# Kernel optimization log

Measured on AMD Instinct MI355X. Metric: run time of the kernel, lower is better.

Reference implementation:

```python
import jax, jax.numpy as jnp
import numpy as np


def _grid_sample_bilinear(img, grid):
    # img: [B,C,H,W]; grid: [B,Hg,Wg,2] normalized to [-1,1] (x,y), align_corners=False,
    # zero padding (torch F.grid_sample defaults).
    B, C, H, W = img.shape
    Hg, Wg = grid.shape[1], grid.shape[2]
    gx, gy = grid[..., 0], grid[..., 1]
    ix = (gx + 1.0) * (W * 0.5) - 0.5
    iy = (gy + 1.0) * (H * 0.5) - 0.5
    ix0 = jnp.floor(ix)
    iy0 = jnp.floor(iy)
    tx = (ix - ix0).reshape(B, 1, -1)
    ty = (iy - iy0).reshape(B, 1, -1)
    img_flat = img.reshape(B, C, H * W)

    def corner(xi, yi):
        valid = ((xi >= 0) & (xi < W) & (yi >= 0) & (yi < H)).reshape(B, 1, -1)
        xc = jnp.clip(xi, 0, W - 1).astype(jnp.int32)
        yc = jnp.clip(yi, 0, H - 1).astype(jnp.int32)
        idx = (yc * W + xc).reshape(B, -1)                      # [B, Hg*Wg]
        vals = jax.vmap(lambda f, i: f[:, i])(img_flat, idx)    # [B, C, Hg*Wg]
        return vals * valid

    v00 = corner(ix0, iy0)
    v01 = corner(ix0 + 1, iy0)
    v10 = corner(ix0, iy0 + 1)
    v11 = corner(ix0 + 1, iy0 + 1)
    out = (v00 * (1 - tx) * (1 - ty) + v01 * tx * (1 - ty)
           + v10 * (1 - tx) * ty + v11 * tx * ty)
    return out.reshape(B, C, Hg, Wg)


def setup_inputs() -> dict:
    key = jax.random.key(0)
    ks = jax.random.split(key, 8)
    B, C, RHO, WP = 32, 384, 25, 256
    HC, WC = 64, 64
    D = 2 * C  # 768, channels after polar/cart concat
    std = 0.02
    return {
        "polar_feat": jax.random.normal(ks[0], (B, C, RHO, WP), jnp.float32),
        "cart_feat": jax.random.normal(ks[1], (B, C, HC, WC), jnp.float32),
        "grid": jax.random.uniform(ks[2], (B, RHO, WP, 2), jnp.float32, -1.0, 1.0),
        "W1_0": jax.random.normal(ks[3], (D, 40), jnp.float32) * std,
        "b1_0": jnp.zeros((40,), jnp.float32),
        "W2_0": jax.random.normal(ks[4], (40, 1), jnp.float32) * std,
        "b2_0": jnp.zeros((1,), jnp.float32),
        "W1s": jax.random.normal(ks[5], (24, D + 1, 40), jnp.float32) * std,
        "b1s": jnp.zeros((24, 40), jnp.float32),
        "W2s": jax.random.normal(ks[6], (24, 40, 1), jnp.float32) * std,
        "b2s": jnp.zeros((24, 1), jnp.float32),
    }


def reference(polar_feat, cart_feat, grid, W1_0, b1_0, W2_0, b2_0, W1s, b1s, W2s, b2s):
    # Polar grid-sample fusion of cartesian features onto the polar grid.
    fe_cart_p = _grid_sample_bilinear(cart_feat, grid)              # [B,C,25,Wp]
    fe_cat_p = jnp.concatenate([polar_feat, fe_cart_p], axis=1)     # [B,768,25,Wp]
    # AdaptiveAvgPool2d((None,1)): mean over width.
    fe = jnp.mean(fe_cat_p, axis=3)                                 # [B,768,25]

    feats = jnp.transpose(fe, (2, 0, 1))                            # [25,B,768]
    gelu = lambda x: jax.nn.gelu(x, approximate=False)

    # Head 0: no recurrent input.
    h0 = gelu(feats[0] @ W1_0 + b1_0)
    out0 = h0 @ W2_0 + b2_0                                         # [B,1]

    # Heads 1..24: concat previous scalar output before first linear (fully_local=False).
    def step(out_prev, xs):
        feat, W1, b1, W2, b2 = xs
        x = jnp.concatenate([feat, out_prev], axis=-1)              # [B,769]
        h = gelu(x @ W1 + b1)
        o = h @ W2 + b2                                             # [B,1]
        return o, o

    _, outs = jax.lax.scan(step, out0, (feats[1:], W1s, b1s, W2s, b2s))
    out = jnp.concatenate([out0[None], outs], axis=0)               # [25,B,1]
    out = jnp.transpose(out[:, :, 0], (1, 0))                       # [B,25]
    return jnp.clip(out, 0.0, jnp.pi)
```

## Files before the change

### kernel.cpp

```cpp
#include <hip/hip_runtime.h>
#include <math.h>

#define B_    32
#define C_    384
#define RHO_  25
#define WP_   256
#define PIX_  4096
#define D_    768
#define HID_  40
#define NROWS (B_*C_*RHO_)
#define FE_N (RHO_*B_*D_)
#define POLARBLK 2048
#define PCH 8
#define WFRAG_B 262144

typedef _Float16 half_t;
typedef __attribute__((ext_vector_type(8))) _Float16 half8;
typedef __attribute__((ext_vector_type(4))) float f32x4;

__device__ __forceinline__ float gelu_exact(float x) {
    return 0.5f * x * (1.f + erff(x * 0.70710678118654752f));
}

__global__ __launch_bounds__(256) void front_kernel(const float* __restrict__ polar,
        const float* __restrict__ grid,
        const float* __restrict__ W1_0, const float* __restrict__ W1s,
        half_t* __restrict__ Wfrag, float* __restrict__ W1T, float* __restrict__ fe) {
    __shared__ float lb[PIX_];
    int tid = threadIdx.x;
    int bid = blockIdx.x;
    if (bid < POLARBLK) {
        int wid = bid * 4 + (tid >> 6);
        int lane = tid & 63;
        const int NW = POLARBLK * 4;
        for (int r0 = wid; r0 < NROWS; r0 += 4 * NW) {
            float s[4];
            #pragma unroll
            for (int k = 0; k < 4; ++k) {
                int r = r0 + k * NW;
                float4 v = (r < NROWS) ? ((const float4*)(polar + (size_t)r * WP_))[lane]
                                       : make_float4(0.f, 0.f, 0.f, 0.f);
                s[k] = v.x + v.y + v.z + v.w;
            }
            #pragma unroll
            for (int m = 32; m >= 1; m >>= 1) {
                #pragma unroll
                for (int k = 0; k < 4; ++k) s[k] += __shfl_xor(s[k], m, 64);
            }
            if (lane == 0) {
                #pragma unroll
                for (int k = 0; k < 4; ++k) {
                    int r = r0 + k * NW;
                    if (r < NROWS) {
                        int rho = r % RHO_, cch = (r / RHO_) % C_, bb = r / (RHO_ * C_);
                        fe[((size_t)(rho * B_ + bb)) * D_ + cch] = s[k] * (1.f / 256.f);
                    }
                }
            }
        }
    } else if (bid < POLARBLK + B_ * RHO_) {
        int bb = bid - POLARBLK;
        for (int i = tid; i < PIX_ / 4; i += 256) ((float4*)lb)[i] = make_float4(0.f, 0.f, 0.f, 0.f);
        __syncthreads();
        int pt = bb * WP_ + tid;
        float2 g = ((const float2*)grid)[pt];
        float ix = (g.x + 1.f) * 32.f - 0.5f;
        float iy = (g.y + 1.f) * 32.f - 0.5f;
        float x0f = floorf(ix), y0f = floorf(iy);
        float fx = ix - x0f, fy = iy - y0f;
        int x0 = (int)x0f, y0 = (int)y0f;
        const float s = 1.f / 256.f;
        if ((unsigned)x0 < 64u) {
            if ((unsigned)y0 < 64u)       atomicAdd(&lb[y0 * 64 + x0],       (1.f - fx) * (1.f - fy) * s);
            if ((unsigned)(y0 + 1) < 64u) atomicAdd(&lb[(y0 + 1) * 64 + x0], (1.f - fx) * fy * s);
        }
        if ((unsigned)(x0 + 1) < 64u) {
            if ((unsigned)y0 < 64u)       atomicAdd(&lb[y0 * 64 + x0 + 1],       fx * (1.f - fy) * s);
            if ((unsigned)(y0 + 1) < 64u) atomicAdd(&lb[(y0 + 1) * 64 + x0 + 1], fx * fy * s);
        }
        __syncthreads();
        int b = bb / RHO_, rho = bb % RHO_;
        int slot_h = (rho < 16) ? 0 : 1;
        int r16 = rho & 15;
        half_t* base = Wfrag + (size_t)b * WFRAG_B;
        for (int i = tid; i < PIX_; i += 256) {
            int t = i >> 5, k = i & 31;
            int kg = k >> 3, ii = k & 7;
            float wv = lb[i];
            half_t h = (half_t)wv;
            size_t idx = ((size_t)(t * 4 + slot_h) * 64 + kg * 16 + r16) * 8 + ii;
            base[idx] = h;
            base[idx + 1024] = (half_t)(wv - (float)h);
        }
    } else if (bid < POLARBLK + B_ * RHO_ + 25) {
        int i = bid - (POLARBLK + B_ * RHO_);
        const float* src = (i == 0) ? W1_0 : (W1s + (size_t)(i - 1) * 769 * HID_);
        float* dst = W1T + (size_t)i * HID_ * D_;
        for (int idx = tid; idx < HID_ * D_; idx += 256) {
            int j = idx / D_, c = idx % D_;
            dst[idx] = src[c * HID_ + j];
        }
    } else {
        int z = bid - (POLARBLK + B_ * RHO_ + 25);
        for (int i = tid; i < 16 * 96; i += 256) {
            int row = z * 16 + (i / 96), e = i % 96;
            ((float4*)fe)[(size_t)row * 192 + 96 + e] = make_float4(0.f, 0.f, 0.f, 0.f);
        }
    }
}

__global__ __launch_bounds__(256) void cart_mfma_kernel(const float* __restrict__ cart,
        const half_t* __restrict__ Wfrag, float* __restrict__ fe) {
    __shared__ float smem[8704];
    int tid = threadIdx.x;
    int bid = blockIdx.x;
    int b  = bid / (6 * PCH);
    int ct = (bid / PCH) % 6;
    int pc = bid % PCH;
    int w = tid >> 6, lane = tid & 63;
    int row16 = lane & 15, kg = lane >> 4;

    const float* xgbase = cart + ((size_t)b * C_ + ct * 64 + w * 16) * PIX_ + pc * 512;
    const half_t* wbase = Wfrag + (size_t)b * WFRAG_B + (size_t)(pc * 16) * 2048 + lane * 8;

    float* xl = smem + w * 2176;
    int srow = lane >> 4;
    int scol = (lane & 15) * 4;

    f32x4 acc0 = {0.f, 0.f, 0.f, 0.f};
    f32x4 acc1 = {0.f, 0.f, 0.f, 0.f};
    float4 sreg[4];
    half8 wf[2][8];

    #pragma unroll
    for (int i = 0; i < 4; ++i)
        sreg[i] = *(const float4*)(xgbase + (size_t)(srow + 4 * i) * PIX_ + scol);
    #pragma unroll
    for (int ks = 0; ks < 2; ++ks)
        #pragma unroll
        for (int s = 0; s < 4; ++s)
            wf[0][ks * 4 + s] = *(const half8*)(wbase + (size_t)(ks * 4 + s) * 512);
    #pragma unroll
    for (int i = 0; i < 4; ++i)
        *(float4*)(&xl[(srow + 4 * i) * 68 + scol]) = sreg[i];
    #pragma unroll
    for (int i = 0; i < 4; ++i)
        sreg[i] = *(const float4*)(xgbase + (size_t)(srow + 4 * i) * PIX_ + 64 + scol);
    #pragma unroll
    for (int ks = 0; ks < 2; ++ks)
        #pragma unroll
        for (int s = 0; s < 4; ++s)
            wf[1][ks * 4 + s] = *(const half8*)(wbase + (size_t)((2 + ks) * 4 + s) * 512);

    #pragma unroll
    for (int t = 0; t < 8; ++t) {
        const int cb = t & 1;
        const float* xb = xl + cb * 1088;
        #pragma unroll
        for (int ks = 0; ks < 2; ++ks) {
            float4 xa = *(const float4*)(xb + row16 * 68 + ks * 32 + kg * 8);
            float4 xc = *(const float4*)(xb + row16 * 68 + ks * 32 + kg * 8 + 4);
            float xs[8] = {xa.x, xa.y, xa.z, xa.w, xc.x, xc.y, xc.z, xc.w};
            half8 ah, al;
            #pragma unroll
            for (int i = 0; i < 8; ++i) {
                half_t h = (half_t)xs[i];
                ah[i] = h;
                al[i] = (half_t)(xs[i] - (float)h);
            }
            acc0 = __builtin_amdgcn_mfma_f32_16x16x32_f16(ah, wf[cb][ks * 4 + 0], acc0, 0, 0, 0);
            acc0 = __builtin_amdgcn_mfma_f32_16x16x32_f16(ah, wf[cb][ks * 4 + 2], acc0, 0, 0, 0);
            acc0 = __builtin_amdgcn_mfma_f32_16x16x32_f16(al, wf[cb][ks * 4 + 0], acc0, 0, 0, 0);
            acc1 = __builtin_amdgcn_mfma_f32_16x16x32_f16(ah, wf[cb][ks * 4 + 1], acc1, 0, 0, 0);
            acc1 = __builtin_amdgcn_mfma_f32_16x16x32_f16(ah, wf[cb][ks * 4 + 3], acc1, 0, 0, 0);
            acc1 = __builtin_amdgcn_mfma_f32_16x16x32_f16(al, wf[cb][ks * 4 + 1], acc1, 0, 0, 0);
        }
        if (t < 7) {
            #pragma unroll
            for (int i = 0; i < 4; ++i)
                *(float4*)(&xl[(cb ^ 1) * 1088 + (srow + 4 * i) * 68 + scol]) = sreg[i];
            if (t < 6) {
                int off = (t + 2) * 64;
                #pragma unroll
                for (int i = 0; i < 4; ++i)
                    sreg[i] = *(const float4*)(xgbase + (size_t)(srow + 4 * i) * PIX_ + off + scol);
                #pragma unroll
                for (int ks = 0; ks < 2; ++ks)
                    #pragma unroll
                    for (int s = 0; s < 4; ++s)
                        wf[cb][ks * 4 + s] = *(const half8*)(wbase + (size_t)(((t + 2) * 2 + ks) * 4 + s) * 512);
            }
        }
    }

    __syncthreads();
    #pragma unroll
    for (int r = 0; r < 4; ++r)
        smem[row16 * 64 + w * 16 + kg * 4 + r] = acc0[r];
    int rho1 = 16 + row16;
    if (rho1 < RHO_) {
        #pragma unroll
        for (int r = 0; r < 4; ++r)
            smem[rho1 * 64 + w * 16 + kg * 4 + r] = acc1[r];
    }
    __syncthreads();
    for (int oi = tid; oi < 1600; oi += 256) {
        int r = oi >> 6, cc = oi & 63;
        atomicAdd(&fe[((size_t)(r * B_ + b)) * D_ + 384 + ct * 64 + cc], smem[oi]);
    }
}

__global__ __launch_bounds__(256) void mlp_pre_kernel(const float* __restrict__ fe,
        const float* __restrict__ W1T, const float* __restrict__ b1_0,
        const float* __restrict__ b1s, float* __restrict__ G) {
    int lane = threadIdx.x & 63;
    int trip = blockIdx.x * 4 + (threadIdx.x >> 6);
    int jh = trip & 1;
    int pair = trip >> 1;
    int i = pair >> 5, b = pair & 31;
    const float4* f4p = (const float4*)(fe + (size_t)(i * B_ + b) * D_);
    float4 f0 = f4p[lane], f1 = f4p[lane + 64], f2 = f4p[lane + 128];
    int j0 = jh * 20;
    #pragma unroll 2
    for (int j = j0; j < j0 + 20; ++j) {
        const float4* w4p = (const float4*)(W1T + ((size_t)i * HID_ + j) * D_);
        float4 w0 = w4p[lane], w1 = w4p[lane + 64], w2 = w4p[lane + 128];
        float s = f0.x*w0.x + f0.y*w0.y + f0.z*w0.z + f0.w*w0.w
                + f1.x*w1.x + f1.y*w1.y + f1.z*w1.z + f1.w*w1.w
                + f2.x*w2.x + f2.y*w2.y + f2.z*w2.z + f2.w*w2.w;
        #pragma unroll
        for (int m = 32; m >= 1; m >>= 1) s += __shfl_xor(s, m, 64);
        if (lane == 0) {
            float bias = (i == 0) ? b1_0[j] : b1s[(i - 1) * HID_ + j];
            G[(size_t)(i * B_ + b) * HID_ + j] = s + bias;
        }
    }
}

__global__ __launch_bounds__(64) void mlp_seq_kernel(const float* __restrict__ G,
        const float* __restrict__ W1s, const float* __restrict__ W2_0,
        const float* __restrict__ b2_0, const float* __restrict__ W2s,
        const float* __restrict__ b2s, float* __restrict__ out) {
    int lane = threadIdx.x;
    int j2 = lane & 31, b = blockIdx.x * 2 + (lane >> 5);
    bool hi = (j2 < 8);
    float g1[25], g2[25], wl1[25], wl2[25], w2a[25], w2b[25], bsc[25];
    #pragma unroll
    for (int i = 0; i < 25; ++i) {
        g1[i] = G[(size_t)(i * B_ + b) * HID_ + j2];
        g2[i] = hi ? G[(size_t)(i * B_ + b) * HID_ + 32 + j2] : 0.f;
    }
    wl1[0] = 0.f; wl2[0] = 0.f;
    w2a[0] = W2_0[j2]; w2b[0] = hi ? W2_0[32 + j2] : 0.f; bsc[0] = b2_0[0];
    #pragma unroll
    for (int i = 1; i < 25; ++i) {
        size_t base = ((size_t)(i - 1) * 769 + 768) * HID_;
        wl1[i] = W1s[base + j2];
        wl2[i] = hi ? W1s[base + 32 + j2] : 0.f;
        w2a[i] = W2s[(i - 1) * HID_ + j2];
        w2b[i] = hi ? W2s[(i - 1) * HID_ + 32 + j2] : 0.f;
        bsc[i] = b2s[i - 1];
    }
    float op = 0.f;
    #pragma unroll
    for (int i = 0; i < 25; ++i) {
        float x1 = g1[i] + op * wl1[i];
        float x2 = g2[i] + op * wl2[i];
        float p = gelu_exact(x1) * w2a[i] + gelu_exact(x2) * w2b[i];
        #pragma unroll
        for (int m = 16; m >= 1; m >>= 1) p += __shfl_xor(p, m, 64);
        float o = p + bsc[i];
        op = o;
        if (j2 == 0) out[b * 25 + i] = fminf(fmaxf(o, 0.f), 3.14159265358979323846f);
    }
}

extern "C" void kernel_launch(void* const* d_in, const int* in_sizes, int n_in,
                              void* d_out, int out_size, void* d_ws, size_t ws_size,
                              hipStream_t stream) {
    const float* polar = (const float*)d_in[0];
    const float* cart  = (const float*)d_in[1];
    const float* grid  = (const float*)d_in[2];
    const float* W1_0  = (const float*)d_in[3];
    const float* b1_0  = (const float*)d_in[4];
    const float* W2_0  = (const float*)d_in[5];
    const float* b2_0  = (const float*)d_in[6];
    const float* W1s   = (const float*)d_in[7];
    const float* b1s   = (const float*)d_in[8];
    const float* W2s   = (const float*)d_in[9];
    const float* b2s   = (const float*)d_in[10];
    float* out = (float*)d_out;

    half_t* Wfrag = (half_t*)d_ws;
    float* fe   = (float*)(Wfrag + (size_t)B_ * WFRAG_B);
    float* G    = fe + (size_t)FE_N;
    float* W1T  = G + (size_t)RHO_ * B_ * HID_;

    front_kernel<<<POLARBLK + B_ * RHO_ + 25 + 50, 256, 0, stream>>>(polar, grid, W1_0, W1s, Wfrag, W1T, fe);
    cart_mfma_kernel<<<B_ * 6 * PCH, 256, 0, stream>>>(cart, Wfrag, fe);
    mlp_pre_kernel<<<(RHO_ * B_ * 2) / 4, 256, 0, stream>>>(fe, W1T, b1_0, b1s, G);
    mlp_seq_kernel<<<B_ / 2, 64, 0, stream>>>(G, W1s, W2_0, b2_0, W2s, b2s, out);
}
```

Measured before the change: 174.6 us.

## Move polar mean reduction into cart MFMA kernel with interleaved block roles

Removes the polar width-mean reduction from the front kernel, leaving a small prep kernel for grid-weight scatter and weight transposes. The polar reduction blocks are interleaved with the cart MFMA blocks in a single launch (3 cart groups and 4 polar groups per 7), so memory-bound polar reads can overlap compute-heavy cart work. This shortens the serialized front stage, at the cost of mixed block types competing for bandwidth and occupancy.

```diff
diff --git a/kernel.cpp b/kernel.cpp
--- a/kernel.cpp
+++ b/kernel.cpp
@@ -10,9 +10,9 @@
 #define HID_  40
 #define NROWS (B_*C_*RHO_)
 #define FE_N (RHO_*B_*D_)
-#define POLARBLK 2048
 #define PCH 8
 #define WFRAG_B 262144
+#define PNW 8192
 
 typedef _Float16 half_t;
 typedef __attribute__((ext_vector_type(8))) _Float16 half8;
@@ -22,47 +22,16 @@
     return 0.5f * x * (1.f + erff(x * 0.70710678118654752f));
 }
 
-__global__ __launch_bounds__(256) void front_kernel(const float* __restrict__ polar,
-        const float* __restrict__ grid,
+__global__ __launch_bounds__(256) void prep_kernel(const float* __restrict__ grid,
         const float* __restrict__ W1_0, const float* __restrict__ W1s,
         half_t* __restrict__ Wfrag, float* __restrict__ W1T, float* __restrict__ fe) {
     __shared__ float lb[PIX_];
     int tid = threadIdx.x;
     int bid = blockIdx.x;
-    if (bid < POLARBLK) {
-        int wid = bid * 4 + (tid >> 6);
-        int lane = tid & 63;
-        const int NW = POLARBLK * 4;
-        for (int r0 = wid; r0 < NROWS; r0 += 4 * NW) {
-            float s[4];
-            #pragma unroll
-            for (int k = 0; k < 4; ++k) {
-                int r = r0 + k * NW;
-                float4 v = (r < NROWS) ? ((const float4*)(polar + (size_t)r * WP_))[lane]
-                                       : make_float4(0.f, 0.f, 0.f, 0.f);
-                s[k] = v.x + v.y + v.z + v.w;
-            }
-            #pragma unroll
-            for (int m = 32; m >= 1; m >>= 1) {
-                #pragma unroll
-                for (int k = 0; k < 4; ++k) s[k] += __shfl_xor(s[k], m, 64);
-            }
-            if (lane == 0) {
-                #pragma unroll
-                for (int k = 0; k < 4; ++k) {
-                    int r = r0 + k * NW;
-                    if (r < NROWS) {
-                        int rho = r % RHO_, cch = (r / RHO_) % C_, bb = r / (RHO_ * C_);
-                        fe[((size_t)(rho * B_ + bb)) * D_ + cch] = s[k] * (1.f / 256.f);
-                    }
-                }
-            }
-        }
-    } else if (bid < POLARBLK + B_ * RHO_) {
-        int bb = bid - POLARBLK;
+    if (bid < B_ * RHO_) {
         for (int i = tid; i < PIX_ / 4; i += 256) ((float4*)lb)[i] = make_float4(0.f, 0.f, 0.f, 0.f);
         __syncthreads();
-        int pt = bb * WP_ + tid;
+        int pt = bid * WP_ + tid;
         float2 g = ((const float2*)grid)[pt];
         float ix = (g.x + 1.f) * 32.f - 0.5f;
         float iy = (g.y + 1.f) * 32.f - 0.5f;
@@ -79,7 +48,7 @@
             if ((unsigned)(y0 + 1) < 64u) atomicAdd(&lb[(y0 + 1) * 64 + x0 + 1], fx * fy * s);
         }
         __syncthreads();
-        int b = bb / RHO_, rho = bb % RHO_;
+        int b = bid / RHO_, rho = bid % RHO_;
         int slot_h = (rho < 16) ? 0 : 1;
         int r16 = rho & 15;
         half_t* base = Wfrag + (size_t)b * WFRAG_B;
@@ -92,8 +61,8 @@
             base[idx] = h;
             base[idx + 1024] = (half_t)(wv - (float)h);
         }
-    } else if (bid < POLARBLK + B_ * RHO_ + 25) {
-        int i = bid - (POLARBLK + B_ * RHO_);
+    } else if (bid < B_ * RHO_ + 25) {
+        int i = bid - B_ * RHO_;
         const float* src = (i == 0) ? W1_0 : (W1s + (size_t)(i - 1) * 769 * HID_);
         float* dst = W1T + (size_t)i * HID_ * D_;
         for (int idx = tid; idx < HID_ * D_; idx += 256) {
@@ -101,7 +70,7 @@
             dst[idx] = src[c * HID_ + j];
         }
     } else {
-        int z = bid - (POLARBLK + B_ * RHO_ + 25);
+        int z = bid - (B_ * RHO_ + 25);
         for (int i = tid; i < 16 * 96; i += 256) {
             int row = z * 16 + (i / 96), e = i % 96;
             ((float4*)fe)[(size_t)row * 192 + 96 + e] = make_float4(0.f, 0.f, 0.f, 0.f);
@@ -109,104 +78,138 @@
     }
 }
 
-__global__ __launch_bounds__(256) void cart_mfma_kernel(const float* __restrict__ cart,
-        const half_t* __restrict__ Wfrag, float* __restrict__ fe) {
+__global__ __launch_bounds__(256) void main_kernel(const float* __restrict__ polar,
+        const float* __restrict__ cart, const half_t* __restrict__ Wfrag,
+        float* __restrict__ fe) {
     __shared__ float smem[8704];
     int tid = threadIdx.x;
-    int bid = blockIdx.x;
-    int b  = bid / (6 * PCH);
-    int ct = (bid / PCH) % 6;
-    int pc = bid % PCH;
+    int o = blockIdx.x >> 3, sub = blockIdx.x & 7;
+    int g = o / 7, r = o % 7;
     int w = tid >> 6, lane = tid & 63;
-    int row16 = lane & 15, kg = lane >> 4;
-
-    const float* xgbase = cart + ((size_t)b * C_ + ct * 64 + w * 16) * PIX_ + pc * 512;
-    const half_t* wbase = Wfrag + (size_t)b * WFRAG_B + (size_t)(pc * 16) * 2048 + lane * 8;
-
-    float* xl = smem + w * 2176;
-    int srow = lane >> 4;
-    int scol = (lane & 15) * 4;
-
-    f32x4 acc0 = {0.f, 0.f, 0.f, 0.f};
-    f32x4 acc1 = {0.f, 0.f, 0.f, 0.f};
-    float4 sreg[4];
-    half8 wf[2][8];
-
-    #pragma unroll
-    for (int i = 0; i < 4; ++i)
-        sreg[i] = *(const float4*)(xgbase + (size_t)(srow + 4 * i) * PIX_ + scol);
-    #pragma unroll
-    for (int ks = 0; ks < 2; ++ks)
-        #pragma unroll
-        for (int s = 0; s < 4; ++s)
-            wf[0][ks * 4 + s] = *(const half8*)(wbase + (size_t)(ks * 4 + s) * 512);
-    #pragma unroll
-    for (int i = 0; i < 4; ++i)
-        *(float4*)(&xl[(srow + 4 * i) * 68 + scol]) = sreg[i];
-    #pragma unroll
-    for (int i = 0; i < 4; ++i)
-        sreg[i] = *(const float4*)(xgbase + (size_t)(srow + 4 * i) * PIX_ + 64 + scol);
-    #pragma unroll
-    for (int ks = 0; ks < 2; ++ks)
-        #pragma unroll
-        for (int s = 0; s < 4; ++s)
-            wf[1][ks * 4 + s] = *(const half8*)(wbase + (size_t)((2 + ks) * 4 + s) * 512);
-
-    #pragma unroll
-    for (int t = 0; t < 8; ++t) {
-        const int cb = t & 1;
-        const float* xb = xl + cb * 1088;
-        #pragma unroll
-        for (int ks = 0; ks < 2; ++ks) {
-            float4 xa = *(const float4*)(xb + row16 * 68 + ks * 32 + kg * 8);
-            float4 xc = *(const float4*)(xb + row16 * 68 + ks * 32 + kg * 8 + 4);
-            float xs[8] = {xa.x, xa.y, xa.z, xa.w, xc.x, xc.y, xc.z, xc.w};
-            half8 ah, al;
-            #pragma unroll
-            for (int i = 0; i < 8; ++i) {
-                half_t h = (half_t)xs[i];
-                ah[i] = h;
-                al[i] = (half_t)(xs[i] - (float)h);
-            }
-            acc0 = __builtin_amdgcn_mfma_f32_16x16x32_f16(ah, wf[cb][ks * 4 + 0], acc0, 0, 0, 0);
-            acc0 = __builtin_amdgcn_mfma_f32_16x16x32_f16(ah, wf[cb][ks * 4 + 2], acc0, 0, 0, 0);
-            acc0 = __builtin_amdgcn_mfma_f32_16x16x32_f16(al, wf[cb][ks * 4 + 0], acc0, 0, 0, 0);
-            acc1 = __builtin_amdgcn_mfma_f32_16x16x32_f16(ah, wf[cb][ks * 4 + 1], acc1, 0, 0, 0);
-            acc1 = __builtin_amdgcn_mfma_f32_16x16x32_f16(ah, wf[cb][ks * 4 + 3], acc1, 0, 0, 0);
-            acc1 = __builtin_amdgcn_mfma_f32_16x16x32_f16(al, wf[cb][ks * 4 + 1], acc1, 0, 0, 0);
-        }
-        if (t < 7) {
-            #pragma unroll
-            for (int i = 0; i < 4; ++i)
-                *(float4*)(&xl[(cb ^ 1) * 1088 + (srow + 4 * i) * 68 + scol]) = sreg[i];
-            if (t < 6) {
-                int off = (t + 2) * 64;
+
+    if (r < 3) {
+        int bid = (g * 3 + r) * 8 + sub;
+        int b  = bid / (6 * PCH);
+        int ct = (bid / PCH) % 6;
+        int pc = bid % PCH;
+        int row16 = lane & 15, kg = lane >> 4;
+
+        const float* xgbase = cart + ((size_t)b * C_ + ct * 64 + w * 16) * PIX_ + pc * 512;
+        const half_t* wbase = Wfrag + (size_t)b * WFRAG_B + (size_t)(pc * 16) * 2048 + lane * 8;
+
+        float* xl = smem + w * 2176;
+        int srow = lane >> 4;
+        int scol = (lane & 15) * 4;
+
+        f32x4 acc0 = {0.f, 0.f, 0.f, 0.f};
+        f32x4 acc1 = {0.f, 0.f, 0.f, 0.f};
+        float4 sreg[4];
+        half8 wf[2][8];
+
+        #pragma unroll
+        for (int i = 0; i < 4; ++i)
+            sreg[i] = *(const float4*)(xgbase + (size_t)(srow + 4 * i) * PIX_ + scol);
+        #pragma unroll
+        for (int ks = 0; ks < 2; ++ks)
+            #pragma unroll
+            for (int s = 0; s < 4; ++s)
+                wf[0][ks * 4 + s] = *(const half8*)(wbase + (size_t)(ks * 4 + s) * 512);
+        #pragma unroll
+        for (int i = 0; i < 4; ++i)
+            *(float4*)(&xl[(srow + 4 * i) * 68 + scol]) = sreg[i];
+        #pragma unroll
+        for (int i = 0; i < 4; ++i)
+            sreg[i] = *(const float4*)(xgbase + (size_t)(srow + 4 * i) * PIX_ + 64 + scol);
+        #pragma unroll
+        for (int ks = 0; ks < 2; ++ks)
+            #pragma unroll
+            for (int s = 0; s < 4; ++s)
+                wf[1][ks * 4 + s] = *(const half8*)(wbase + (size_t)((2 + ks) * 4 + s) * 512);
+
+        #pragma unroll
+        for (int t = 0; t < 8; ++t) {
+            const int cb = t & 1;
+            const float* xb = xl + cb * 1088;
+            #pragma unroll
+            for (int ks = 0; ks < 2; ++ks) {
+                float4 xa = *(const float4*)(xb + row16 * 68 + ks * 32 + kg * 8);
+                float4 xc = *(const float4*)(xb + row16 * 68 + ks * 32 + kg * 8 + 4);
+                float xs[8] = {xa.x, xa.y, xa.z, xa.w, xc.x, xc.y, xc.z, xc.w};
+                half8 ah, al;
+                #pragma unroll
+                for (int i = 0; i < 8; ++i) {
+                    half_t h = (half_t)xs[i];
+                    ah[i] = h;
+                    al[i] = (half_t)(xs[i] - (float)h);
+                }
+                acc0 = __builtin_amdgcn_mfma_f32_16x16x32_f16(ah, wf[cb][ks * 4 + 0], acc0, 0, 0, 0);
+                acc0 = __builtin_amdgcn_mfma_f32_16x16x32_f16(ah, wf[cb][ks * 4 + 2], acc0, 0, 0, 0);
+                acc0 = __builtin_amdgcn_mfma_f32_16x16x32_f16(al, wf[cb][ks * 4 + 0], acc0, 0, 0, 0);
+                acc1 = __builtin_amdgcn_mfma_f32_16x16x32_f16(ah, wf[cb][ks * 4 + 1], acc1, 0, 0, 0);
+                acc1 = __builtin_amdgcn_mfma_f32_16x16x32_f16(ah, wf[cb][ks * 4 + 3], acc1, 0, 0, 0);
+                acc1 = __builtin_amdgcn_mfma_f32_16x16x32_f16(al, wf[cb][ks * 4 + 1], acc1, 0, 0, 0);
+            }
+            if (t < 7) {
                 #pragma unroll
                 for (int i = 0; i < 4; ++i)
-                    sreg[i] = *(const float4*)(xgbase + (size_t)(srow + 4 * i) * PIX_ + off + scol);
+                    *(float4*)(&xl[(cb ^ 1) * 1088 + (srow + 4 * i) * 68 + scol]) = sreg[i];
+                if (t < 6) {
+                    int off = (t + 2) * 64;
+                    #pragma unroll
+                    for (int i = 0; i < 4; ++i)
+                        sreg[i] = *(const float4*)(xgbase + (size_t)(srow + 4 * i) * PIX_ + off + scol);
+                    #pragma unroll
+                    for (int ks = 0; ks < 2; ++ks)
+                        #pragma unroll
+                        for (int s = 0; s < 4; ++s)
+                            wf[cb][ks * 4 + s] = *(const half8*)(wbase + (size_t)(((t + 2) * 2 + ks) * 4 + s) * 512);
+                }
+            }
+        }
+
+        __syncthreads();
+        #pragma unroll
+        for (int rr = 0; rr < 4; ++rr)
+            smem[row16 * 64 + w * 16 + kg * 4 + rr] = acc0[rr];
+        int rho1 = 16 + row16;
+        if (rho1 < RHO_) {
+            #pragma unroll
+            for (int rr = 0; rr < 4; ++rr)
+                smem[rho1 * 64 + w * 16 + kg * 4 + rr] = acc1[rr];
+        }
+        __syncthreads();
+        for (int oi = tid; oi < 1600; oi += 256) {
+            int rr = oi >> 6, cc = oi & 63;
+            atomicAdd(&fe[((size_t)(rr * B_ + b)) * D_ + 384 + ct * 64 + cc], smem[oi]);
+        }
+    } else {
+        int pid = (g * 4 + (r - 3)) * 8 + sub;
+        int wid = pid * 4 + w;
+        for (int r0 = wid; r0 < NROWS; r0 += 4 * PNW) {
+            float s[4];
+            #pragma unroll
+            for (int k = 0; k < 4; ++k) {
+                int rr = r0 + k * PNW;
+                float4 v = (rr < NROWS) ? ((const float4*)(polar + (size_t)rr * WP_))[lane]
+                                        : make_float4(0.f, 0.f, 0.f, 0.f);
+                s[k] = v.x + v.y + v.z + v.w;
+            }
+            #pragma unroll
+            for (int m = 32; m >= 1; m >>= 1) {
                 #pragma unroll
-                for (int ks = 0; ks < 2; ++ks)
-                    #pragma unroll
-                    for (int s = 0; s < 4; ++s)
-                        wf[cb][ks * 4 + s] = *(const half8*)(wbase + (size_t)(((t + 2) * 2 + ks) * 4 + s) * 512);
-            }
-        }
-    }
-
-    __syncthreads();
-    #pragma unroll
-    for (int r = 0; r < 4; ++r)
-        smem[row16 * 64 + w * 16 + kg * 4 + r] = acc0[r];
-    int rho1 = 16 + row16;
-    if (rho1 < RHO_) {
-        #pragma unroll
-        for (int r = 0; r < 4; ++r)
-            smem[rho1 * 64 + w * 16 + kg * 4 + r] = acc1[r];
-    }
-    __syncthreads();
-    for (int oi = tid; oi < 1600; oi += 256) {
-        int r = oi >> 6, cc = oi & 63;
-        atomicAdd(&fe[((size_t)(r * B_ + b)) * D_ + 384 + ct * 64 + cc], smem[oi]);
+                for (int k = 0; k < 4; ++k) s[k] += __shfl_xor(s[k], m, 64);
+            }
+            if (lane == 0) {
+                #pragma unroll
+                for (int k = 0; k < 4; ++k) {
+                    int rr = r0 + k * PNW;
+                    if (rr < NROWS) {
+                        int rho = rr % RHO_, cch = (rr / RHO_) % C_, bb = rr / (RHO_ * C_);
+                        fe[((size_t)(rho * B_ + bb)) * D_ + cch] = s[k] * (1.f / 256.f);
+                    }
+                }
+            }
+        }
     }
 }
 
@@ -296,8 +299,8 @@
     float* G    = fe + (size_t)FE_N;
     float* W1T  = G + (size_t)RHO_ * B_ * HID_;
 
-    front_kernel<<<POLARBLK + B_ * RHO_ + 25 + 50, 256, 0, stream>>>(polar, grid, W1_0, W1s, Wfrag, W1T, fe);
-    cart_mfma_kernel<<<B_ * 6 * PCH, 256, 0, stream>>>(cart, Wfrag, fe);
+    prep_kernel<<<B_ * RHO_ + 25 + 50, 256, 0, stream>>>(grid, W1_0, W1s, Wfrag, W1T, fe);
+    main_kernel<<<3584, 256, 0, stream>>>(polar, cart, Wfrag, fe);
     mlp_pre_kernel<<<(RHO_ * B_ * 2) / 4, 256, 0, stream>>>(fe, W1T, b1_0, b1s, G);
     mlp_seq_kernel<<<B_ / 2, 64, 0, stream>>>(G, W1s, W2_0, b2_0, W2s, b2s, out);
 }
```

After: 193.4 us. +10.7%, slower.
